# Kernel optimization log

Hardware: AMD Instinct MI355X
Metric: run time of the kernel (lower is better)

## Reference

```python
import jax, jax.numpy as jnp
import numpy as np

B, S, D, E, H = 4, 4096, 1024, 8, 128  # batch, seq, d_model, experts, expert hidden (hardcoded 128)


def setup_inputs() -> dict:
    key = jax.random.key(0)
    ks = jax.random.split(key, 7)
    s_in = 1.0 / np.sqrt(D)
    s_h = 1.0 / np.sqrt(H)
    return {
        "x": jax.random.normal(ks[0], (B, S, D), dtype=jnp.float32),
        "W1": jax.random.normal(ks[1], (E, D, H), dtype=jnp.float32) * s_in,
        "b1": jax.random.normal(ks[2], (E, H), dtype=jnp.float32) * s_in,
        "W2": jax.random.normal(ks[3], (E, H, D), dtype=jnp.float32) * s_h,
        "b2": jax.random.normal(ks[4], (E, D), dtype=jnp.float32) * s_h,
        "Wg": jax.random.normal(ks[5], (D, E), dtype=jnp.float32) * s_in,
        "bg": jax.random.normal(ks[6], (E,), dtype=jnp.float32) * s_in,
    }


def reference(x, W1, b1, W2, b2, Wg, bg):
    # Gate: softmax over experts. [B,S,E]
    gate = jax.nn.softmax(jnp.einsum("bsd,de->bse", x, Wg) + bg, axis=-1)
    # Dense per-expert MLP applied to every token.
    h = jax.nn.relu(jnp.einsum("bsd,edh->bseh", x, W1) + b1)          # [B,S,E,H]
    y = jnp.einsum("bseh,eho->bseo", h, W2) + b2                       # [B,S,E,D]
    # Fused weighted sum over the expert axis (replaces the python double loop).
    out = jnp.einsum("bse,bseo->bso", gate, y)                         # [B,S,D]
    return out
```

## Files before the change

kernel.cpp:

```cpp
#include <hip/hip_runtime.h>
#include <hip/hip_bf16.h>

#define B_ 4
#define S_ 4096
#define D_ 1024
#define E_ 8
#define H_ 128
#define M_ (B_*S_)
#define K_ 1024
#define N_ 1024
#define NT_ (K_/64)
#define NIT_ (NT_/2)

typedef short bf16x8 __attribute__((ext_vector_type(8)));
typedef float f32x4 __attribute__((ext_vector_type(4)));

__device__ __forceinline__ unsigned short f2bf(float f){
  union { float f; unsigned int u; } v; v.f = f;
  unsigned int u = v.u;
  unsigned int r = (u + 0x7fffu + ((u >> 16) & 1u)) >> 16;
  return (unsigned short)r;
}

__device__ __forceinline__ void gload16(const void* g, void* l){
  __builtin_amdgcn_global_load_lds((const __attribute__((address_space(1))) void*)g,
                                   (__attribute__((address_space(3))) void*)l, 16, 0, 0);
}

__global__ __launch_bounds__(256)
void prep_x_gate(const float* __restrict__ x, const float* __restrict__ Wg,
                 const float* __restrict__ bg, unsigned short* __restrict__ xb,
                 float* __restrict__ gate){
  int tid = threadIdx.x;
  int lane = tid & 63;
  int m = blockIdx.x * 4 + (tid >> 6);
  const float* xr = x + (size_t)m * D_;
  unsigned short* xbr = xb + (size_t)m * D_;
  float acc[E_];
  #pragma unroll
  for (int e = 0; e < E_; ++e) acc[e] = 0.f;
  #pragma unroll
  for (int c = 0; c < D_/64; ++c){
    int d = c*64 + lane;
    float xs = xr[d];
    xbr[d] = f2bf(xs);
    const float4 w0 = *(const float4*)(Wg + (size_t)d * E_);
    const float4 w1 = *(const float4*)(Wg + (size_t)d * E_ + 4);
    acc[0] = fmaf(xs, w0.x, acc[0]); acc[1] = fmaf(xs, w0.y, acc[1]);
    acc[2] = fmaf(xs, w0.z, acc[2]); acc[3] = fmaf(xs, w0.w, acc[3]);
    acc[4] = fmaf(xs, w1.x, acc[4]); acc[5] = fmaf(xs, w1.y, acc[5]);
    acc[6] = fmaf(xs, w1.z, acc[6]); acc[7] = fmaf(xs, w1.w, acc[7]);
  }
  #pragma unroll
  for (int off = 32; off > 0; off >>= 1){
    #pragma unroll
    for (int e = 0; e < E_; ++e) acc[e] += __shfl_xor(acc[e], off, 64);
  }
  float lg[E_]; float mx = -1e30f;
  #pragma unroll
  for (int e = 0; e < E_; ++e){ lg[e] = acc[e] + bg[e]; mx = fmaxf(mx, lg[e]); }
  float s = 0.f;
  #pragma unroll
  for (int e = 0; e < E_; ++e){ lg[e] = expf(lg[e] - mx); s += lg[e]; }
  float inv = 1.f / s;
  if (lane < E_) gate[(size_t)m * E_ + lane] = lg[lane] * inv;
}

__global__ __launch_bounds__(256)
void transpose_pack(const float* __restrict__ in, unsigned short* __restrict__ out,
                    int C, int ostride, int in_estride, int out_ebase){
  __shared__ float t[32][33];
  int e = blockIdx.z;
  const float* ip = in + (size_t)e * in_estride;
  unsigned short* op = out + (size_t)e * out_ebase;
  int tx = threadIdx.x, ty = threadIdx.y;
  int c0 = blockIdx.x * 32, r0 = blockIdx.y * 32;
  #pragma unroll
  for (int yy = 0; yy < 32; yy += 8)
    t[ty + yy][tx] = ip[(size_t)(r0 + ty + yy) * C + (c0 + tx)];
  __syncthreads();
  #pragma unroll
  for (int yy = 0; yy < 32; yy += 8)
    op[(size_t)(c0 + ty + yy) * ostride + (r0 + tx)] = f2bf(t[tx][ty + yy]);
}

#define READ_A(b,r) do{ int ab_ = (b)*16384 + abase0; \
  _Pragma("unroll") for (int f2 = 0; f2 < 4; ++f2){ \
    af[f2][0] = *(const bf16x8*)&lds[ab_ + ((r)*4+f2)*1024 + bk0]; \
    af[f2][1] = *(const bf16x8*)&lds[ab_ + ((r)*4+f2)*1024 + bk1]; } }while(0)
#define READ_B(b,c) do{ int bb_ = (b)*16384 + bbase0; \
  _Pragma("unroll") for (int j2 = 0; j2 < 2; ++j2){ \
    bfr[(c)*2+j2][0] = *(const bf16x8*)&lds[bb_ + ((c)*2+j2)*1024 + bk0]; \
    bfr[(c)*2+j2][1] = *(const bf16x8*)&lds[bb_ + ((c)*2+j2)*1024 + bk1]; } }while(0)
#define MFMA16(r,c) do{ \
  _Pragma("unroll") for (int f2 = 0; f2 < 4; ++f2) \
  _Pragma("unroll") for (int j2 = 0; j2 < 2; ++j2){ \
    acc[(r)*4+f2][(c)*2+j2] = __builtin_amdgcn_mfma_f32_16x16x32_bf16(af[f2][0], bfr[(c)*2+j2][0], acc[(r)*4+f2][(c)*2+j2], 0,0,0); \
    acc[(r)*4+f2][(c)*2+j2] = __builtin_amdgcn_mfma_f32_16x16x32_bf16(af[f2][1], bfr[(c)*2+j2][1], acc[(r)*4+f2][(c)*2+j2], 0,0,0); \
  } }while(0)
#define PH_MID  __builtin_amdgcn_s_barrier(); \
                __builtin_amdgcn_s_setprio(1)
#define PH_END  __builtin_amdgcn_s_setprio(0)
#define VMW(N)  asm volatile("s_waitcnt vmcnt(" #N ")" ::: "memory")

template<int PASS>
__global__ __launch_bounds__(512, 2)
void gemm_moe8(const unsigned short* __restrict__ A,
               const unsigned short* __restrict__ Bt,
               const float* __restrict__ gate,
               const float* __restrict__ bias,
               void* __restrict__ outp)
{
  __shared__ unsigned short lds[65536];

  int bid = blockIdx.x;
  int xcd = bid & 7, pos = bid >> 3;
  int mb = xcd * 8 + (pos >> 2);
  int nb = pos & 3;
  int m0 = mb * 256, n0 = nb * 256;

  int tid = threadIdx.x;
  int lane = tid & 63;
  int w = tid >> 6;
  int wm = w & 1, wn = w >> 1;
  int rowi = lane & 15, s4 = lane >> 4;

  int sg = (tid & 7) ^ ((tid >> 3) & 7);
  const unsigned short* gA = A  + (size_t)(m0 + (tid >> 3)) * K_ + sg * 8;
  const unsigned short* gB = Bt + (size_t)(n0 + (tid >> 3)) * K_ + sg * 8;
  int t8 = tid * 8;

#define STAGE_A(b,h,kt) do{ const unsigned short* g_ = gA + (size_t)((h)*128)*K_ + (kt)*64; \
  gload16(g_,                 &lds[(b)*16384 + (h)*8192 + t8]); \
  gload16(g_ + (size_t)64*K_, &lds[(b)*16384 + (h)*8192 + t8 + 4096]); }while(0)
#define STAGE_B(b,h,kt) do{ const unsigned short* g_ = gB + (size_t)((h)*128)*K_ + (kt)*64; \
  gload16(g_,                 &lds[32768 + (b)*16384 + (h)*8192 + t8]); \
  gload16(g_ + (size_t)64*K_, &lds[32768 + (b)*16384 + (h)*8192 + t8 + 4096]); }while(0)

  int bk0 = rowi*64 + (( s4     ) ^ (rowi & 7)) * 8;
  int bk1 = rowi*64 + ((4 + s4  ) ^ (rowi & 7)) * 8;
  int abase0 = wm * 8192;
  int bbase0 = 32768 + (wn >> 1) * 8192 + (wn & 1) * 4096;

  f32x4 acc[8][4];
  #pragma unroll
  for (int i = 0; i < 8; ++i){
    #pragma unroll
    for (int j = 0; j < 4; ++j){ f32x4 z = {0.f,0.f,0.f,0.f}; acc[i][j] = z; }
  }
  bf16x8 af[4][2], bfr[4][2];

  STAGE_B(0,0,0); STAGE_B(0,1,0);
  STAGE_A(0,0,0); STAGE_A(0,1,0);
  STAGE_B(1,0,1); STAGE_B(1,1,1);
  STAGE_A(1,0,1);
  VMW(6);
  __builtin_amdgcn_s_barrier();

  #pragma unroll 1
  for (int it = 0; it < NIT_; ++it){
    int kt1  = 2*it + 1;
    int ktn0 = 2*it + 2, ktn1 = 2*it + 3;
    bool more = (it < NIT_ - 1);
    READ_A(0,0); READ_B(0,0);
    STAGE_A(1,1,kt1);
    PH_MID; MFMA16(0,0); PH_END;
    READ_B(0,1);
    PH_MID; MFMA16(0,1); PH_END;
    READ_A(0,1);
    if (more) STAGE_B(0,0,ktn0);
    PH_MID; MFMA16(1,1); PH_END;
    if (more){ STAGE_B(0,1,ktn0); VMW(4); }
    else     { VMW(0); }
    PH_MID; MFMA16(1,0); PH_END;
    READ_A(1,0); READ_B(1,0);
    if (more) STAGE_A(0,0,ktn0);
    PH_MID; MFMA16(0,0); PH_END;
    READ_B(1,1);
    if (more) STAGE_A(0,1,ktn0);
    PH_MID; MFMA16(0,1); PH_END;
    READ_A(1,1);
    if (more) STAGE_B(1,0,ktn1);
    PH_MID; MFMA16(1,1); PH_END;
    if (more){ STAGE_B(1,1,ktn1); STAGE_A(1,0,ktn1); }
    VMW(6);
    PH_MID; MFMA16(1,0); PH_END;
  }

  int ncol0 = n0 + wn*64;
  if (PASS == 1){
    __builtin_amdgcn_s_barrier();
    unsigned short* Hp = (unsigned short*)outp;
    float* lws = (float*)lds + w * 4096;
    int e = nb*2 + (wn >> 1);
    float b1v[4];
    #pragma unroll
    for (int j = 0; j < 4; ++j) b1v[j] = bias[e*H_ + (wn&1)*64 + j*16 + rowi];
    #pragma unroll
    for (int ci = 0; ci < 2; ++ci){
      #pragma unroll
      for (int f2 = 0; f2 < 4; ++f2){
        int fi = ci*4 + f2;
        #pragma unroll
        for (int jj = 0; jj < 4; ++jj){
          int m = m0 + wm*128 + fi*16 + s4*4 + jj;
          float g = gate[(size_t)m*E_ + e];
          int r_l = f2*16 + s4*4 + jj;
          #pragma unroll
          for (int j = 0; j < 4; ++j){
            float v = fmaxf(acc[fi][j][jj] + b1v[j], 0.f) * g;
            lws[r_l*64 + ((j*16 + rowi) ^ (s4 << 4))] = v;
          }
        }
      }
      asm volatile("s_waitcnt lgkmcnt(0)" ::: "memory");
      #pragma unroll
      for (int it2 = 0; it2 < 16; ++it2){
        int r_l = it2*4 + (lane >> 4);
        int c4  = lane & 15;
        int X2  = it2 & 3;
        f32x4 v = *(const f32x4*)&lws[r_l*64 + ((c4*4) ^ (X2 << 4))];
        union { unsigned short us[4]; uint2 u2; } pk;
        #pragma unroll
        for (int q = 0; q < 4; ++q) pk.us[q] = f2bf(v[q]);
        int m = m0 + wm*128 + ci*64 + r_l;
        *(uint2*)&Hp[(size_t)m*N_ + ncol0 + c4*4] = pk.u2;
      }
      if (ci == 0) asm volatile("s_waitcnt lgkmcnt(0)" ::: "memory");
    }
  } else {
    float* Out = (float*)outp;
    float b2v[8][4];
    #pragma unroll
    for (int j = 0; j < 4; ++j){
      int n = ncol0 + j*16 + rowi;
      #pragma unroll
      for (int e = 0; e < 8; ++e) b2v[e][j] = bias[(size_t)e*N_ + n];
    }
    #pragma unroll
    for (int fi = 0; fi < 8; ++fi){
      #pragma unroll
      for (int jj = 0; jj < 4; ++jj){
        int m = m0 + wm*128 + fi*16 + s4*4 + jj;
        const float4 g0 = *(const float4*)(gate + (size_t)m*E_);
        const float4 g1 = *(const float4*)(gate + (size_t)m*E_ + 4);
        float bv[4];
        #pragma unroll
        for (int j = 0; j < 4; ++j)
          bv[j] = g0.x*b2v[0][j] + g0.y*b2v[1][j] + g0.z*b2v[2][j] + g0.w*b2v[3][j]
                + g1.x*b2v[4][j] + g1.y*b2v[5][j] + g1.z*b2v[6][j] + g1.w*b2v[7][j];
        #pragma unroll
        for (int j = 0; j < 4; ++j)
          Out[(size_t)m*N_ + ncol0 + j*16 + rowi] = acc[fi][j][jj] + bv[j];
      }
    }
  }
#undef STAGE_A
#undef STAGE_B
}

extern "C" void kernel_launch(void* const* d_in, const int* in_sizes, int n_in,
                              void* d_out, int out_size, void* d_ws, size_t ws_size,
                              hipStream_t stream){
  const float* x  = (const float*)d_in[0];
  const float* W1 = (const float*)d_in[1];
  const float* b1 = (const float*)d_in[2];
  const float* W2 = (const float*)d_in[3];
  const float* b2 = (const float*)d_in[4];
  const float* Wg = (const float*)d_in[5];
  const float* bg = (const float*)d_in[6];
  float* out = (float*)d_out;

  char* ws = (char*)d_ws;
  unsigned short* xb  = (unsigned short*)(ws);
  unsigned short* Hp  = (unsigned short*)(ws + ((size_t)32<<20));
  unsigned short* B1T = (unsigned short*)(ws + ((size_t)64<<20));
  unsigned short* B2T = (unsigned short*)(ws + ((size_t)66<<20));
  float*          gate= (float*)(ws + ((size_t)68<<20));

  hipLaunchKernelGGL(prep_x_gate, dim3(M_/4), dim3(256), 0, stream, x, Wg, bg, xb, gate);
  hipLaunchKernelGGL(transpose_pack, dim3(128/32, 1024/32, 8), dim3(32,8), 0, stream,
                     W1, B1T, 128, 1024, 1024*128, 128*1024);
  hipLaunchKernelGGL(transpose_pack, dim3(1024/32, 128/32, 8), dim3(32,8), 0, stream,
                     W2, B2T, 1024, 1024, 128*1024, 128);
  hipLaunchKernelGGL((gemm_moe8<1>), dim3(256), dim3(512), 0, stream,
                     xb, B1T, gate, b1, (void*)Hp);
  hipLaunchKernelGGL((gemm_moe8<2>), dim3(256), dim3(512), 0, stream,
                     Hp, B2T, gate, b2, (void*)out);
}
```

Measured before the change: 101.3 us.

## Process eight rows per wave in gate prep with transpose-style reduction

Each wavefront in the x-conversion and gate kernel now handles eight token rows instead of one. Each Wg load is reused across those eight rows. The 64 partial sums are reduced with a recursive-halving butterfly, so each lane ends up owning one (row, expert) logit, and the softmax runs with 8-lane shuffles. This is meant to cut redundant Wg loads and shuffle-reduction work per token, at the cost of higher register pressure (64 accumulators) and one eighth as many blocks.

```diff
diff --git a/kernel.cpp b/kernel.cpp
--- a/kernel.cpp
+++ b/kernel.cpp
@@ -33,37 +33,55 @@
                  float* __restrict__ gate){
   int tid = threadIdx.x;
   int lane = tid & 63;
-  int m = blockIdx.x * 4 + (tid >> 6);
-  const float* xr = x + (size_t)m * D_;
-  unsigned short* xbr = xb + (size_t)m * D_;
-  float acc[E_];
-  #pragma unroll
-  for (int e = 0; e < E_; ++e) acc[e] = 0.f;
+  int m0 = (blockIdx.x * 4 + (tid >> 6)) * 8;
+  const float* xr = x + (size_t)m0 * D_;
+  unsigned short* xbr = xb + (size_t)m0 * D_;
+
+  float vv[64];
+  #pragma unroll
+  for (int i = 0; i < 64; ++i) vv[i] = 0.f;
+
   #pragma unroll
   for (int c = 0; c < D_/64; ++c){
     int d = c*64 + lane;
-    float xs = xr[d];
-    xbr[d] = f2bf(xs);
     const float4 w0 = *(const float4*)(Wg + (size_t)d * E_);
     const float4 w1 = *(const float4*)(Wg + (size_t)d * E_ + 4);
-    acc[0] = fmaf(xs, w0.x, acc[0]); acc[1] = fmaf(xs, w0.y, acc[1]);
-    acc[2] = fmaf(xs, w0.z, acc[2]); acc[3] = fmaf(xs, w0.w, acc[3]);
-    acc[4] = fmaf(xs, w1.x, acc[4]); acc[5] = fmaf(xs, w1.y, acc[5]);
-    acc[6] = fmaf(xs, w1.z, acc[6]); acc[7] = fmaf(xs, w1.w, acc[7]);
-  }
-  #pragma unroll
-  for (int off = 32; off > 0; off >>= 1){
-    #pragma unroll
-    for (int e = 0; e < E_; ++e) acc[e] += __shfl_xor(acc[e], off, 64);
-  }
-  float lg[E_]; float mx = -1e30f;
-  #pragma unroll
-  for (int e = 0; e < E_; ++e){ lg[e] = acc[e] + bg[e]; mx = fmaxf(mx, lg[e]); }
-  float s = 0.f;
-  #pragma unroll
-  for (int e = 0; e < E_; ++e){ lg[e] = expf(lg[e] - mx); s += lg[e]; }
-  float inv = 1.f / s;
-  if (lane < E_) gate[(size_t)m * E_ + lane] = lg[lane] * inv;
+    #pragma unroll
+    for (int t = 0; t < 8; ++t){
+      float xs = xr[(size_t)t*D_ + d];
+      xbr[(size_t)t*D_ + d] = f2bf(xs);
+      vv[t*8+0] = fmaf(xs, w0.x, vv[t*8+0]);
+      vv[t*8+1] = fmaf(xs, w0.y, vv[t*8+1]);
+      vv[t*8+2] = fmaf(xs, w0.z, vv[t*8+2]);
+      vv[t*8+3] = fmaf(xs, w0.w, vv[t*8+3]);
+      vv[t*8+4] = fmaf(xs, w1.x, vv[t*8+4]);
+      vv[t*8+5] = fmaf(xs, w1.y, vv[t*8+5]);
+      vv[t*8+6] = fmaf(xs, w1.z, vv[t*8+6]);
+      vv[t*8+7] = fmaf(xs, w1.w, vv[t*8+7]);
+    }
+  }
+
+  #pragma unroll
+  for (int r = 0; r < 6; ++r){
+    int hi = (lane >> r) & 1;
+    #pragma unroll
+    for (int j = 0; j < (32 >> r); ++j){
+      float a = vv[2*j], b = vv[2*j+1];
+      float send = hi ? a : b;
+      float recv = __shfl_xor(send, 1 << r, 64);
+      vv[j] = (hi ? b : a) + recv;
+    }
+  }
+
+  float lg = vv[0] + bg[lane & 7];
+  float mx = lg;
+  #pragma unroll
+  for (int o = 1; o < 8; o <<= 1) mx = fmaxf(mx, __shfl_xor(mx, o, 64));
+  float ex = expf(lg - mx);
+  float s = ex;
+  #pragma unroll
+  for (int o = 1; o < 8; o <<= 1) s += __shfl_xor(s, o, 64);
+  gate[(size_t)m0 * E_ + lane] = ex / s;
 }
 
 __global__ __launch_bounds__(256)
@@ -278,7 +296,7 @@
   unsigned short* B2T = (unsigned short*)(ws + ((size_t)66<<20));
   float*          gate= (float*)(ws + ((size_t)68<<20));
 
-  hipLaunchKernelGGL(prep_x_gate, dim3(M_/4), dim3(256), 0, stream, x, Wg, bg, xb, gate);
+  hipLaunchKernelGGL(prep_x_gate, dim3(M_/32), dim3(256), 0, stream, x, Wg, bg, xb, gate);
   hipLaunchKernelGGL(transpose_pack, dim3(128/32, 1024/32, 8), dim3(32,8), 0, stream,
                      W1, B1T, 128, 1024, 1024*128, 128*1024);
   hipLaunchKernelGGL(transpose_pack, dim3(1024/32, 128/32, 8), dim3(32,8), 0, stream,
```

After: 102.8 us. No clear change (+1.5%).
